# Kernel tuning notes

Hardware: AMD Instinct MI355X
Metric: run time of the kernel (lower is better)

The kernel has to match this reference:

```python
import jax, jax.numpy as jnp
import numpy as np

N_STEPS = 16
T_FINAL = 1.0


def setup_inputs() -> dict:
    key = jax.random.key(0)
    k = jax.random.split(key, 5)
    B, n, S = 131072, 8, 1
    return {
        "U0": jax.random.normal(k[0], (B, n, n), jnp.float32),
        "eps": jax.random.normal(k[1], (S, B, n, n), jnp.float32),
        "W0": 0.1 * jax.random.normal(k[2], (n, n), jnp.float32),
        "W1": 0.1 * jax.random.normal(k[3], (n, n), jnp.float32),
        "W2": 0.1 * jax.random.normal(k[4], (n, n), jnp.float32),
    }


def _alg_dyn(t, U, W0, W1, W2):
    # F(t, U; p) = antisym(W0 + t*W1 + U W2 U^T)  (real anti-Hermitian part)
    M = W0 + t * W1 + jnp.einsum('bij,jk,blk->bil', U, W2, U)
    return 0.5 * (M - jnp.swapaxes(M, -1, -2))


def _vel(t, U, W0, W1, W2):
    # dU/dt = F(t, U) @ U
    return _alg_dyn(t, U, W0, W1, W2) @ U


def _logj_rate(t, U, eps, W0, W1, W2):
    # Hutchinson estimator of tr(d vel / dU) per batch element: E_v[v . J v]
    f = lambda u: _vel(t, u, W0, W1, W2)

    def one(v):
        _, jv = jax.jvp(f, (U,), (v,))
        return jnp.sum(v * jv, axis=(-2, -1))  # [B]

    return jnp.mean(jax.vmap(one)(eps), axis=0)  # [B]


def reference(U0, eps, W0, W1, W2):
    dt = T_FINAL / N_STEPS

    def rhs(t, U):
        return _vel(t, U, W0, W1, W2), _logj_rate(t, U, eps, W0, W1, W2)

    def step(carry, i):
        U, lj = carry
        t = i.astype(U.dtype) * dt
        k1u, k1l = rhs(t, U)
        k2u, k2l = rhs(t + 0.5 * dt, U + 0.5 * dt * k1u)
        k3u, k3l = rhs(t + 0.5 * dt, U + 0.5 * dt * k2u)
        k4u, k4l = rhs(t + dt, U + dt * k3u)
        U = U + (dt / 6.0) * (k1u + 2.0 * k2u + 2.0 * k3u + k4u)
        lj = lj + (dt / 6.0) * (k1l + 2.0 * k2l + 2.0 * k3l + k4l)
        return (U, lj), None

    logj0 = jnp.zeros((U0.shape[0],), U0.dtype)
    (U, logj), _ = jax.lax.scan(step, (U0, logj0), jnp.arange(N_STEPS))
    return U, logj
```

## Files before the change

### kernel.cpp

```cpp
#include <hip/hip_runtime.h>
#include <stdint.h>

typedef unsigned int u32;
typedef unsigned short u16;
typedef _Float16 h2 __attribute__((ext_vector_type(2)));

#define NSTEP 16
#define DTS (1.0f/16.0f)

#define TAB_FLAG 0
#define TAB_W2M  8
#define TAB_W2C  72
#define TAB_WT   112

__device__ __forceinline__ float b2f(u16 h){ return __uint_as_float(((u32)h) << 16); }
__device__ __forceinline__ float bflo(u32 w){ return __uint_as_float(w << 16); }
__device__ __forceinline__ float bfhi(u32 w){ return __uint_as_float(w & 0xffff0000u); }
__device__ __forceinline__ u32 f2b(float f){
  u32 u = __float_as_uint(f);
  return (u + 0x7fffu + ((u >> 16) & 1u)) >> 16;
}
__host__ __device__ constexpr int TRI(int i, int j){ return i*7 - (i*(i-1))/2 + (j-i-1); }

__device__ __forceinline__ u32 pkh(float a, float b){
  return __builtin_bit_cast(u32, __builtin_amdgcn_cvt_pkrtz(a, b));
}
__device__ __forceinline__ float dot8h(const u32* a, const u32* b){
  float s = __builtin_amdgcn_fdot2(__builtin_bit_cast(h2, a[0]), __builtin_bit_cast(h2, b[0]), 0.0f, false);
  s = __builtin_amdgcn_fdot2(__builtin_bit_cast(h2, a[1]), __builtin_bit_cast(h2, b[1]), s, false);
  s = __builtin_amdgcn_fdot2(__builtin_bit_cast(h2, a[2]), __builtin_bit_cast(h2, b[2]), s, false);
  s = __builtin_amdgcn_fdot2(__builtin_bit_cast(h2, a[3]), __builtin_bit_cast(h2, b[3]), s, false);
  return s;
}
__device__ __forceinline__ float Fel(const float* Fu, int i, int k){
  if (i == k) return 0.0f;
  return (i < k) ? Fu[TRI(i,k)] : -Fu[TRI(k,i)];
}

__global__ void prep_kernel(const void* __restrict__ W0v, const void* __restrict__ W1v,
                            const void* __restrict__ W2v, float* __restrict__ ws)
{
  __shared__ int sflag;
  __shared__ float sW0[64], sW1[64], sW2[64];
  int t = threadIdx.x;

  if (t == 0) {
    const u16* w2h = (const u16*)W2v;
    int ok = 1;
    for (int x = 0; x < 64; ++x) {
      float v = b2f(w2h[x]);
      if (!(v > -1024.0f && v < 1024.0f)) { ok = 0; break; }
    }
    sflag = ok;
    ws[TAB_FLAG] = (float)ok;
  }
  __syncthreads();
  int isbf = sflag;

  if (t < 64) {
    if (isbf) {
      sW0[t] = b2f(((const u16*)W0v)[t]);
      sW1[t] = b2f(((const u16*)W1v)[t]);
      sW2[t] = b2f(((const u16*)W2v)[t]);
    } else {
      sW0[t] = ((const float*)W0v)[t];
      sW1[t] = ((const float*)W1v)[t];
      sW2[t] = ((const float*)W2v)[t];
    }
  }
  __syncthreads();

  if (t < 64) {
    int i = t >> 3, j = t & 7;
    ws[TAB_W2M + t] = sW2[t] - sW2[j*8+i];
  }
  if (t < 32) {
    int j = t >> 2, kk = t & 3;
    ((u32*)ws)[TAB_W2C + t] = pkh(sW2[(2*kk)*8 + j], sW2[(2*kk+1)*8 + j]);
  }
  for (int idx = t; idx < 64*28; idx += 256) {
    int s = idx / 28;
    int e = idx - s*28;
    int i = 0, r = e;
    while (r >= 7 - i) { r -= 7 - i; ++i; }
    int j = i + 1 + r;
    int step = s >> 2, st = s & 3;
    float toff = (st == 0) ? 0.0f : ((st == 3) ? 1.0f : 0.5f);
    float tt = ((float)step + toff) * DTS;
    float w0a = 0.5f*(sW0[i*8+j] - sW0[j*8+i]);
    float w1a = 0.5f*(sW1[i*8+j] - sW1[j*8+i]);
    ws[TAB_WT + s*32 + e] = fmaf(tt, w1a, w0a);
  }
}

__global__ void __attribute__((amdgpu_flat_work_group_size(256,256), amdgpu_waves_per_eu(1,1)))
flow_kernel(const void* __restrict__ U0v, const void* __restrict__ EPSv,
            const float* __restrict__ ws, void* __restrict__ outv, int B)
{
  const int b = blockIdx.x * 256 + threadIdx.x;
  if (b >= B) return;
  const int isbf = (ws[TAB_FLAG] != 0.0f);

  float U[64];
  u32 Vh[32], Eh[32];

  {
    float V[64];
    if (isbf) {
      const uint4* pu = (const uint4*)((const u16*)U0v + (size_t)b*64);
      const uint4* pv = (const uint4*)((const u16*)EPSv + (size_t)b*64);
      #pragma unroll
      for (int q = 0; q < 8; ++q) {
        uint4 xu = pu[q];
        uint4 xv = pv[q];
        U[8*q+0]=bflo(xu.x); U[8*q+1]=bfhi(xu.x);
        U[8*q+2]=bflo(xu.y); U[8*q+3]=bfhi(xu.y);
        U[8*q+4]=bflo(xu.z); U[8*q+5]=bfhi(xu.z);
        U[8*q+6]=bflo(xu.w); U[8*q+7]=bfhi(xu.w);
        V[8*q+0]=bflo(xv.x); V[8*q+1]=bfhi(xv.x);
        V[8*q+2]=bflo(xv.y); V[8*q+3]=bfhi(xv.y);
        V[8*q+4]=bflo(xv.z); V[8*q+5]=bfhi(xv.z);
        V[8*q+6]=bflo(xv.w); V[8*q+7]=bfhi(xv.w);
      }
    } else {
      const float4* pu = (const float4*)((const float*)U0v + (size_t)b*64);
      const float4* pv = (const float4*)((const float*)EPSv + (size_t)b*64);
      #pragma unroll
      for (int q = 0; q < 16; ++q) {
        float4 xu = pu[q];
        float4 xv = pv[q];
        U[4*q+0]=xu.x; U[4*q+1]=xu.y; U[4*q+2]=xu.z; U[4*q+3]=xu.w;
        V[4*q+0]=xv.x; V[4*q+1]=xv.y; V[4*q+2]=xv.z; V[4*q+3]=xv.w;
      }
    }
    const float* M = ws + TAB_W2M;
    #pragma unroll
    for (int i = 0; i < 8; ++i) {
      float e[8];
      #pragma unroll
      for (int j = 0; j < 8; ++j) {
        float s = V[i*8+0] * M[0*8+j];
        #pragma unroll
        for (int k = 1; k < 8; ++k) s = fmaf(V[i*8+k], M[k*8+j], s);
        e[j] = s;
      }
      #pragma unroll
      for (int kk = 0; kk < 4; ++kk) {
        Vh[i*4+kk] = pkh(V[i*8+2*kk], V[i*8+2*kk+1]);
        Eh[i*4+kk] = pkh(e[2*kk], e[2*kk+1]);
      }
    }
  }

  u32 w2c[32];
  #pragma unroll
  for (int x = 0; x < 32; ++x) w2c[x] = ((const u32*)ws)[TAB_W2C + x];

  float lj = 0.0f;

  #pragma unroll 1
  for (int step = 0; step < NSTEP; ++step) {
    float Us[64], acc[64];
    #pragma unroll
    for (int x = 0; x < 64; ++x) { Us[x] = U[x]; acc[x] = 0.0f; }

    #pragma unroll 1
    for (int stage = 0; stage < 4; ++stage) {
      const float* wt = ws + TAB_WT + (size_t)(((step << 2) | stage) << 5);

      u32 Uh[32];
      #pragma unroll
      for (int e = 0; e < 32; ++e) Uh[e] = pkh(U[2*e], U[2*e+1]);

      float Dp[28], Gp[28];
      float Ssum = 0.0f;
      #pragma unroll
      for (int r = 0; r < 8; ++r) {
        #pragma unroll
        for (int m = 0; m < 8; ++m) {
          if (m == r) continue;
          float dv = dot8h(Vh + r*4, Uh + m*4);
          float de = dot8h(Eh + r*4, Uh + m*4);
          if (m > r) {
            Dp[TRI(r,m)] = dv;
            Gp[TRI(r,m)] = de;
          } else {
            Ssum = fmaf(Dp[TRI(m,r)] - dv, Gp[TRI(m,r)] - de, Ssum);
          }
        }
      }
      float cl = (stage == 1 || stage == 2) ? (DTS/6.0f) : (DTS/12.0f);
      lj = fmaf(cl, Ssum, lj);

      float Fu[28];
      #pragma unroll
      for (int r = 0; r < 8; ++r) {
        float ar[8];
        #pragma unroll
        for (int j = 0; j < 8; ++j) ar[j] = dot8h(Uh + r*4, w2c + j*4);
        u32 Ah[4];
        #pragma unroll
        for (int kk = 0; kk < 4; ++kk) Ah[kk] = pkh(ar[2*kk], ar[2*kk+1]);
        #pragma unroll
        for (int j = 0; j < 8; ++j) {
          if (j == r) continue;
          float da = dot8h(Ah, Uh + j*4);
          if (j > r) Fu[TRI(r,j)] = fmaf(0.5f, da, wt[TRI(r,j)]);
          else       Fu[TRI(j,r)] = fmaf(-0.5f, da, Fu[TRI(j,r)]);
        }
      }

      u32 Fh[32], Uc[32];
      #pragma unroll
      for (int i = 0; i < 8; ++i)
        #pragma unroll
        for (int kk = 0; kk < 4; ++kk)
          Fh[i*4+kk] = pkh(Fel(Fu, i, 2*kk), Fel(Fu, i, 2*kk+1));
      #pragma unroll
      for (int j = 0; j < 8; ++j)
        #pragma unroll
        for (int kk = 0; kk < 4; ++kk)
          Uc[j*4+kk] = pkh(U[(2*kk)*8+j], U[(2*kk+1)*8+j]);

      float wa = (stage == 1 || stage == 2) ? 2.0f : 1.0f;
      float cs = (stage == 2) ? DTS : (0.5f*DTS);
      #pragma unroll
      for (int i = 0; i < 8; ++i) {
        #pragma unroll
        for (int j = 0; j < 8; ++j) {
          float kv = dot8h(Fh + i*4, Uc + j*4);
          acc[i*8+j] = fmaf(wa, kv, acc[i*8+j]);
          if (stage < 3) U[i*8+j] = fmaf(cs, kv, Us[i*8+j]);
        }
      }
    }

    #pragma unroll
    for (int x = 0; x < 64; ++x) U[x] = fmaf(DTS/6.0f, acc[x], Us[x]);
  }

  if (isbf) {
    u16* outU = (u16*)outv;
    uint4* po = (uint4*)(outU + (size_t)b*64);
    #pragma unroll
    for (int q = 0; q < 8; ++q) {
      uint4 o;
      o.x = f2b(U[8*q+0]) | (f2b(U[8*q+1]) << 16);
      o.y = f2b(U[8*q+2]) | (f2b(U[8*q+3]) << 16);
      o.z = f2b(U[8*q+4]) | (f2b(U[8*q+5]) << 16);
      o.w = f2b(U[8*q+6]) | (f2b(U[8*q+7]) << 16);
      po[q] = o;
    }
    outU[(size_t)B*64 + b] = (u16)f2b(lj);
  } else {
    float* outU = (float*)outv;
    float4* po = (float4*)(outU + (size_t)b*64);
    #pragma unroll
    for (int q = 0; q < 16; ++q) {
      float4 o;
      o.x = U[4*q+0]; o.y = U[4*q+1]; o.z = U[4*q+2]; o.w = U[4*q+3];
      po[q] = o;
    }
    outU[(size_t)B*64 + b] = lj;
  }
}

extern "C" void kernel_launch(void* const* d_in, const int* in_sizes, int n_in,
                              void* d_out, int out_size, void* d_ws, size_t ws_size,
                              hipStream_t stream) {
  const void* U0  = d_in[0];
  const void* EPS = d_in[1];
  const void* W0  = d_in[2];
  const void* W1  = d_in[3];
  const void* W2  = d_in[4];
  float* ws = (float*)d_ws;
  int B = in_sizes[0] / 64;

  hipLaunchKernelGGL(prep_kernel, dim3(1), dim3(256), 0, stream, W0, W1, W2, ws);
  hipLaunchKernelGGL(flow_kernel, dim3((B + 255) / 256), dim3(256), 0, stream,
                     U0, EPS, ws, d_out, B);
}
```

Baseline: 623.4 us.

## Move V/E half vectors to LDS and cut registers for two waves per EU

The packed half-precision probe vectors V and E move from registers into a per-block shared-memory array with a strided layout, and are reloaded each stage. Fp32 U is replaced by packed-half Uh updated in place, and the transposed Uc is built by bit shuffling instead of conversions. The Hutchinson term is computed from a single difference array D, and the waves-per-EU hint rises from 1 to 2. The aim is to cut VGPR pressure so more waves can hide latency, at the cost of extra LDS reads each stage and 64KB of LDS per block, which may itself limit occupancy.

```diff
diff --git a/kernel.cpp b/kernel.cpp
--- a/kernel.cpp
+++ b/kernel.cpp
@@ -3,7 +3,6 @@
 
 typedef unsigned int u32;
 typedef unsigned short u16;
-typedef _Float16 h2 __attribute__((ext_vector_type(2)));
 
 #define NSTEP 16
 #define DTS (1.0f/16.0f)
@@ -12,6 +11,9 @@
 #define TAB_W2M  8
 #define TAB_W2C  72
 #define TAB_WT   112
+
+typedef _Float16 f16;
+typedef f16 h2 __attribute__((ext_vector_type(2)));
 
 __device__ __forceinline__ float b2f(u16 h){ return __uint_as_float(((u32)h) << 16); }
 __device__ __forceinline__ float bflo(u32 w){ return __uint_as_float(w << 16); }
@@ -25,11 +27,13 @@
 __device__ __forceinline__ u32 pkh(float a, float b){
   return __builtin_bit_cast(u32, __builtin_amdgcn_cvt_pkrtz(a, b));
 }
+__device__ __forceinline__ h2 u2h(u32 x){ return __builtin_bit_cast(h2, x); }
+
 __device__ __forceinline__ float dot8h(const u32* a, const u32* b){
-  float s = __builtin_amdgcn_fdot2(__builtin_bit_cast(h2, a[0]), __builtin_bit_cast(h2, b[0]), 0.0f, false);
-  s = __builtin_amdgcn_fdot2(__builtin_bit_cast(h2, a[1]), __builtin_bit_cast(h2, b[1]), s, false);
-  s = __builtin_amdgcn_fdot2(__builtin_bit_cast(h2, a[2]), __builtin_bit_cast(h2, b[2]), s, false);
-  s = __builtin_amdgcn_fdot2(__builtin_bit_cast(h2, a[3]), __builtin_bit_cast(h2, b[3]), s, false);
+  float s = __builtin_amdgcn_fdot2(u2h(a[0]), u2h(b[0]), 0.0f, false);
+  s = __builtin_amdgcn_fdot2(u2h(a[1]), u2h(b[1]), s, false);
+  s = __builtin_amdgcn_fdot2(u2h(a[2]), u2h(b[2]), s, false);
+  s = __builtin_amdgcn_fdot2(u2h(a[3]), u2h(b[3]), s, false);
   return s;
 }
 __device__ __forceinline__ float Fel(const float* Fu, int i, int k){
@@ -93,16 +97,18 @@
   }
 }
 
-__global__ void __attribute__((amdgpu_flat_work_group_size(256,256), amdgpu_waves_per_eu(1,1)))
+__global__ void __attribute__((amdgpu_flat_work_group_size(256,256), amdgpu_waves_per_eu(2)))
 flow_kernel(const void* __restrict__ U0v, const void* __restrict__ EPSv,
             const float* __restrict__ ws, void* __restrict__ outv, int B)
 {
-  const int b = blockIdx.x * 256 + threadIdx.x;
+  __shared__ uint2 ve[256*32];
+  const int tid = threadIdx.x;
+  const int b = blockIdx.x * 256 + tid;
+  uint2* myve = &ve[((tid >> 6) << 11) + (tid & 63)];
   if (b >= B) return;
   const int isbf = (ws[TAB_FLAG] != 0.0f);
 
-  float U[64];
-  u32 Vh[32], Eh[32];
+  float Us[64];
 
   {
     float V[64];
@@ -113,10 +119,10 @@
       for (int q = 0; q < 8; ++q) {
         uint4 xu = pu[q];
         uint4 xv = pv[q];
-        U[8*q+0]=bflo(xu.x); U[8*q+1]=bfhi(xu.x);
-        U[8*q+2]=bflo(xu.y); U[8*q+3]=bfhi(xu.y);
-        U[8*q+4]=bflo(xu.z); U[8*q+5]=bfhi(xu.z);
-        U[8*q+6]=bflo(xu.w); U[8*q+7]=bfhi(xu.w);
+        Us[8*q+0]=bflo(xu.x); Us[8*q+1]=bfhi(xu.x);
+        Us[8*q+2]=bflo(xu.y); Us[8*q+3]=bfhi(xu.y);
+        Us[8*q+4]=bflo(xu.z); Us[8*q+5]=bfhi(xu.z);
+        Us[8*q+6]=bflo(xu.w); Us[8*q+7]=bfhi(xu.w);
         V[8*q+0]=bflo(xv.x); V[8*q+1]=bfhi(xv.x);
         V[8*q+2]=bflo(xv.y); V[8*q+3]=bfhi(xv.y);
         V[8*q+4]=bflo(xv.z); V[8*q+5]=bfhi(xv.z);
@@ -129,7 +135,7 @@
       for (int q = 0; q < 16; ++q) {
         float4 xu = pu[q];
         float4 xv = pv[q];
-        U[4*q+0]=xu.x; U[4*q+1]=xu.y; U[4*q+2]=xu.z; U[4*q+3]=xu.w;
+        Us[4*q+0]=xu.x; Us[4*q+1]=xu.y; Us[4*q+2]=xu.z; Us[4*q+3]=xu.w;
         V[4*q+0]=xv.x; V[4*q+1]=xv.y; V[4*q+2]=xv.z; V[4*q+3]=xv.w;
       }
     }
@@ -144,11 +150,10 @@
         for (int k = 1; k < 8; ++k) s = fmaf(V[i*8+k], M[k*8+j], s);
         e[j] = s;
       }
-      #pragma unroll
-      for (int kk = 0; kk < 4; ++kk) {
-        Vh[i*4+kk] = pkh(V[i*8+2*kk], V[i*8+2*kk+1]);
-        Eh[i*4+kk] = pkh(e[2*kk], e[2*kk+1]);
-      }
+      myve[(2*i+0)*64]  = make_uint2(pkh(V[i*8+0],V[i*8+1]), pkh(V[i*8+2],V[i*8+3]));
+      myve[(2*i+1)*64]  = make_uint2(pkh(V[i*8+4],V[i*8+5]), pkh(V[i*8+6],V[i*8+7]));
+      myve[(16+2*i)*64] = make_uint2(pkh(e[0],e[1]), pkh(e[2],e[3]));
+      myve[(17+2*i)*64] = make_uint2(pkh(e[4],e[5]), pkh(e[6],e[7]));
     }
   }
 
@@ -160,33 +165,43 @@
 
   #pragma unroll 1
   for (int step = 0; step < NSTEP; ++step) {
-    float Us[64], acc[64];
-    #pragma unroll
-    for (int x = 0; x < 64; ++x) { Us[x] = U[x]; acc[x] = 0.0f; }
+    float acc[64];
+    u32 Uh[32];
+    #pragma unroll
+    for (int x = 0; x < 32; ++x) {
+      Uh[x] = pkh(Us[2*x], Us[2*x+1]);
+      acc[2*x] = 0.0f; acc[2*x+1] = 0.0f;
+    }
 
     #pragma unroll 1
     for (int stage = 0; stage < 4; ++stage) {
       const float* wt = ws + TAB_WT + (size_t)(((step << 2) | stage) << 5);
 
-      u32 Uh[32];
-      #pragma unroll
-      for (int e = 0; e < 32; ++e) Uh[e] = pkh(U[2*e], U[2*e+1]);
-
-      float Dp[28], Gp[28];
-      float Ssum = 0.0f;
+      float D[28];
       #pragma unroll
       for (int r = 0; r < 8; ++r) {
+        uint2 va = myve[(2*r+0)*64];
+        uint2 vb = myve[(2*r+1)*64];
+        u32 vr[4] = {va.x, va.y, vb.x, vb.y};
         #pragma unroll
         for (int m = 0; m < 8; ++m) {
           if (m == r) continue;
-          float dv = dot8h(Vh + r*4, Uh + m*4);
-          float de = dot8h(Eh + r*4, Uh + m*4);
-          if (m > r) {
-            Dp[TRI(r,m)] = dv;
-            Gp[TRI(r,m)] = de;
-          } else {
-            Ssum = fmaf(Dp[TRI(m,r)] - dv, Gp[TRI(m,r)] - de, Ssum);
-          }
+          float dv = dot8h(vr, Uh + m*4);
+          if (m > r) D[TRI(r,m)] = dv;
+          else       D[TRI(m,r)] -= dv;
+        }
+      }
+      float Ssum = 0.0f;
+      #pragma unroll
+      for (int r = 0; r < 8; ++r) {
+        uint2 ea = myve[(16+2*r)*64];
+        uint2 eb = myve[(17+2*r)*64];
+        u32 er[4] = {ea.x, ea.y, eb.x, eb.y};
+        #pragma unroll
+        for (int m = 0; m < 8; ++m) {
+          if (m == r) continue;
+          float de = dot8h(er, Uh + m*4);
+          Ssum = fmaf(de, (m > r) ? D[TRI(r,m)] : -D[TRI(m,r)], Ssum);
         }
       }
       float cl = (stage == 1 || stage == 2) ? (DTS/6.0f) : (DTS/12.0f);
@@ -210,33 +225,40 @@
         }
       }
 
-      u32 Fh[32], Uc[32];
-      #pragma unroll
-      for (int i = 0; i < 8; ++i)
-        #pragma unroll
-        for (int kk = 0; kk < 4; ++kk)
-          Fh[i*4+kk] = pkh(Fel(Fu, i, 2*kk), Fel(Fu, i, 2*kk+1));
-      #pragma unroll
-      for (int j = 0; j < 8; ++j)
-        #pragma unroll
-        for (int kk = 0; kk < 4; ++kk)
-          Uc[j*4+kk] = pkh(U[(2*kk)*8+j], U[(2*kk+1)*8+j]);
+      u32 Uc[32];
+      #pragma unroll
+      for (int kk = 0; kk < 4; ++kk) {
+        #pragma unroll
+        for (int jh = 0; jh < 4; ++jh) {
+          u32 A  = Uh[(2*kk)*4 + jh];
+          u32 Bv = Uh[(2*kk+1)*4 + jh];
+          Uc[(2*jh+0)*4 + kk] = (A & 0xffffu) | (Bv << 16);
+          Uc[(2*jh+1)*4 + kk] = (A >> 16) | (Bv & 0xffff0000u);
+        }
+      }
 
       float wa = (stage == 1 || stage == 2) ? 2.0f : 1.0f;
       float cs = (stage == 2) ? DTS : (0.5f*DTS);
       #pragma unroll
       for (int i = 0; i < 8; ++i) {
+        u32 Fh[4];
+        #pragma unroll
+        for (int kk = 0; kk < 4; ++kk) Fh[kk] = pkh(Fel(Fu, i, 2*kk), Fel(Fu, i, 2*kk+1));
+        float un[8];
         #pragma unroll
         for (int j = 0; j < 8; ++j) {
-          float kv = dot8h(Fh + i*4, Uc + j*4);
+          float kv = dot8h(Fh, Uc + j*4);
           acc[i*8+j] = fmaf(wa, kv, acc[i*8+j]);
-          if (stage < 3) U[i*8+j] = fmaf(cs, kv, Us[i*8+j]);
-        }
-      }
-    }
-
-    #pragma unroll
-    for (int x = 0; x < 64; ++x) U[x] = fmaf(DTS/6.0f, acc[x], Us[x]);
+          un[j] = fmaf(cs, kv, Us[i*8+j]);
+        }
+        if (stage < 3) {
+          #pragma unroll
+          for (int kk = 0; kk < 4; ++kk) Uh[i*4+kk] = pkh(un[2*kk], un[2*kk+1]);
+        }
+      }
+    }
+    #pragma unroll
+    for (int x = 0; x < 64; ++x) Us[x] = fmaf(DTS/6.0f, acc[x], Us[x]);
   }
 
   if (isbf) {
@@ -245,10 +267,10 @@
     #pragma unroll
     for (int q = 0; q < 8; ++q) {
       uint4 o;
-      o.x = f2b(U[8*q+0]) | (f2b(U[8*q+1]) << 16);
-      o.y = f2b(U[8*q+2]) | (f2b(U[8*q+3]) << 16);
-      o.z = f2b(U[8*q+4]) | (f2b(U[8*q+5]) << 16);
-      o.w = f2b(U[8*q+6]) | (f2b(U[8*q+7]) << 16);
+      o.x = f2b(Us[8*q+0]) | (f2b(Us[8*q+1]) << 16);
+      o.y = f2b(Us[8*q+2]) | (f2b(Us[8*q+3]) << 16);
+      o.z = f2b(Us[8*q+4]) | (f2b(Us[8*q+5]) << 16);
+      o.w = f2b(Us[8*q+6]) | (f2b(Us[8*q+7]) << 16);
       po[q] = o;
     }
     outU[(size_t)B*64 + b] = (u16)f2b(lj);
@@ -257,9 +279,7 @@
     float4* po = (float4*)(outU + (size_t)b*64);
     #pragma unroll
     for (int q = 0; q < 16; ++q) {
-      float4 o;
-      o.x = U[4*q+0]; o.y = U[4*q+1]; o.z = U[4*q+2]; o.w = U[4*q+3];
-      po[q] = o;
+      po[q] = make_float4(Us[4*q+0], Us[4*q+1], Us[4*q+2], Us[4*q+3]);
     }
     outU[(size_t)B*64 + b] = lj;
   }
```

New measurement: 1.069 ms. +71.5%, slower.
